# Kernel optimization log

Hardware: AMD Instinct MI355X
Metric: run time of the kernel (lower is better)

The kernel has to match this reference:

```python
import jax, jax.numpy as jnp
import numpy as np

N_NODES = 100000
N_EDGES = 3200000
D_IN = 128
D_H0 = 64
D_H1 = 32
N_GRAPHS = 1024
N_CLASSES = 16


def setup_inputs() -> dict:
    key = jax.random.key(0)
    ks = jax.random.split(key, 9)
    x = jax.random.normal(ks[0], (N_NODES, D_IN), dtype=jnp.float32)
    edge_index = jax.random.randint(ks[1], (2, N_EDGES), 0, N_NODES, dtype=jnp.int64)
    node_graph_index = jnp.sort(
        jax.random.randint(ks[2], (N_NODES,), 0, N_GRAPHS, dtype=jnp.int64))

    def glorot(k, shape):
        lim = np.sqrt(6.0 / (shape[0] + shape[1]))
        return jax.random.uniform(k, shape, jnp.float32, -lim, lim)

    W0 = glorot(ks[3], (D_IN, D_H0))
    b0 = jnp.zeros((D_H0,), jnp.float32)
    W1 = glorot(ks[4], (D_H0, D_H1))
    b1 = jnp.zeros((D_H1,), jnp.float32)
    Wd = glorot(ks[5], (D_H1, N_CLASSES))
    bd = jnp.zeros((N_CLASSES,), jnp.float32)
    return {"x": x, "edge_index": edge_index, "node_graph_index": node_graph_index,
            "W0": W0, "b0": b0, "W1": W1, "b1": b1, "Wd": Wd, "bd": bd}


def reference(x, edge_index, node_graph_index, W0, b0, W1, b1, Wd, bd):
    N = x.shape[0]
    # GCN renormalization: add self-loops, symmetric D^-1/2 (A+I) D^-1/2
    loops = jnp.arange(N, dtype=edge_index.dtype)
    row = jnp.concatenate([edge_index[0], loops])  # target nodes
    col = jnp.concatenate([edge_index[1], loops])  # source nodes
    deg = jax.ops.segment_sum(jnp.ones_like(row, dtype=x.dtype), row, num_segments=N)
    inv_sqrt = jax.lax.rsqrt(deg)  # deg >= 1 thanks to self-loops
    norm = inv_sqrt[row] * inv_sqrt[col]  # [E+N]

    def gcn(h, W, b):
        hW = h @ W                                   # [N, d_out]
        msg = hW[col] * norm[:, None]                # [E+N, d_out]
        agg = jax.ops.segment_sum(msg, row, num_segments=N)
        return jax.nn.relu(agg + b)

    h = gcn(x, W0, b0)          # [N, 64]  (dropout is identity at inference)
    h = gcn(h, W1, b1)          # [N, 32]

    # mean pool over graphs
    sums = jax.ops.segment_sum(h, node_graph_index, num_segments=N_GRAPHS)
    cnt = jax.ops.segment_sum(jnp.ones((N,), x.dtype), node_graph_index,
                              num_segments=N_GRAPHS)
    pooled = sums / jnp.maximum(cnt, 1.0)[:, None]   # [G, 32]
    return pooled @ Wd + bd                          # [G, n_classes]
```

## Files before the change

### kernel.cpp

```cpp
#include <hip/hip_runtime.h>

#define BSHIFT 7
#define BSIZE 128
#define MAXB 1024
#define CHUNK 4096
#define CAP 4608

typedef unsigned short bfraw;

__device__ __forceinline__ bfraw f2bf(float f) {
    unsigned u = __float_as_uint(f);
    unsigned r = u + 0x7FFFu + ((u >> 16) & 1u);
    return (bfraw)(r >> 16);
}
__device__ __forceinline__ float bflo(unsigned u) { return __uint_as_float(u << 16); }
__device__ __forceinline__ float bfhi(unsigned u) { return __uint_as_float(u & 0xFFFF0000u); }


__global__ __launch_bounds__(1024) void k_binit(int* __restrict__ bcur, int nbuckets) {
    int b = threadIdx.x;
    if (b < nbuckets) bcur[b] = b * CAP;
}

__global__ __launch_bounds__(512) void k_bscatter(const int* __restrict__ row,
                                                  const int* __restrict__ col,
                                                  int* __restrict__ bcur,
                                                  int* __restrict__ bedge,
                                                  int E, int nbuckets) {
    __shared__ int h[MAXB];
    __shared__ int base[MAXB];
    int tid = threadIdx.x;
    for (int i = tid; i < nbuckets; i += 512) h[i] = 0;
    __syncthreads();
    int start = blockIdx.x * CHUNK;
    int end = min(E, start + CHUNK);
    for (int i = start + tid; i < end; i += 512)
        atomicAdd(&h[row[i] >> BSHIFT], 1);
    __syncthreads();
    for (int i = tid; i < nbuckets; i += 512) {
        int c = h[i];
        base[i] = c ? atomicAdd(&bcur[i], c) : 0;
        h[i] = 0;
    }
    __syncthreads();
    for (int i = start + tid; i < end; i += 512) {
        int r = row[i], c = col[i];
        int b = r >> BSHIFT;
        int p = base[b] + atomicAdd(&h[b], 1);
        if (p < (b + 1) * CAP)
            bedge[p] = ((r & (BSIZE - 1)) << 17) | c;
    }
}

__global__ __launch_bounds__(512) void k_bexact(const int* __restrict__ bedge,
                                                const int* __restrict__ bcur,
                                                int* __restrict__ off,
                                                int* __restrict__ off2,
                                                int* __restrict__ scol,
                                                float* __restrict__ invs, int N) {
    __shared__ int sedge[CAP];
    __shared__ int ldeg[BSIZE];
    __shared__ int lex[BSIZE];
    int b = blockIdx.x;
    int tid = threadIdx.x;
    int nstart = b << BSHIFT;
    int ncount = min(BSIZE, N - nstart);
    int s = b * CAP;
    int cntE = min(bcur[b] - s, CAP);
    for (int k = tid; k < cntE; k += 512) sedge[k] = bedge[s + k];
    if (tid < BSIZE) ldeg[tid] = 0;
    __syncthreads();
    for (int k = tid; k < cntE; k += 512)
        atomicAdd(&ldeg[sedge[k] >> 17], 1);
    __syncthreads();
    if (tid < BSIZE) lex[tid] = ldeg[tid];
    __syncthreads();
    for (int d = 1; d < BSIZE; d <<= 1) {
        int a = 0;
        if (tid < BSIZE && tid >= d) a = lex[tid - d];
        __syncthreads();
        if (tid < BSIZE) lex[tid] += a;
        __syncthreads();
    }
    if (tid < BSIZE) lex[tid] -= ldeg[tid];
    __syncthreads();
    if (tid < ncount) {
        int node = nstart + tid;
        int st = s + lex[tid];
        off[node] = st;
        off2[node] = st + ldeg[tid];
        invs[node] = rsqrtf((float)(ldeg[tid] + 1));
    }
    if (tid < BSIZE) ldeg[tid] = 0;
    __syncthreads();
    for (int k = tid; k < cntE; k += 512) {
        int p = sedge[k];
        int lr = p >> 17;
        int pos = s + lex[lr] + atomicAdd(&ldeg[lr], 1);
        scol[pos] = p & 0x1FFFF;
    }
}


__global__ __launch_bounds__(256) void k_gemm0(const float* __restrict__ x,
                                               const float* __restrict__ W,
                                               const float* __restrict__ invs,
                                               bfraw* __restrict__ out, int N) {
    __shared__ float sW[128 * 64];
    for (int i = threadIdx.x; i < 2048; i += 256)
        ((float4*)sW)[i] = ((const float4*)W)[i];
    __syncthreads();
    int t = threadIdx.x;
    int tc = t & 15, tr = t >> 4;
    int rbase = blockIdx.x * 64 + tr * 4;
    float acc[4][4] = {};
    int rr[4];
#pragma unroll
    for (int i = 0; i < 4; ++i) rr[i] = min(rbase + i, N - 1);
    for (int k = 0; k < 128; k += 4) {
        float4 wv0 = *(const float4*)&sW[(k + 0) * 64 + tc * 4];
        float4 wv1 = *(const float4*)&sW[(k + 1) * 64 + tc * 4];
        float4 wv2 = *(const float4*)&sW[(k + 2) * 64 + tc * 4];
        float4 wv3 = *(const float4*)&sW[(k + 3) * 64 + tc * 4];
#pragma unroll
        for (int i = 0; i < 4; ++i) {
            float4 xv = *(const float4*)(x + (size_t)rr[i] * 128 + k);
            acc[i][0] = fmaf(xv.x, wv0.x, acc[i][0]);
            acc[i][1] = fmaf(xv.x, wv0.y, acc[i][1]);
            acc[i][2] = fmaf(xv.x, wv0.z, acc[i][2]);
            acc[i][3] = fmaf(xv.x, wv0.w, acc[i][3]);
            acc[i][0] = fmaf(xv.y, wv1.x, acc[i][0]);
            acc[i][1] = fmaf(xv.y, wv1.y, acc[i][1]);
            acc[i][2] = fmaf(xv.y, wv1.z, acc[i][2]);
            acc[i][3] = fmaf(xv.y, wv1.w, acc[i][3]);
            acc[i][0] = fmaf(xv.z, wv2.x, acc[i][0]);
            acc[i][1] = fmaf(xv.z, wv2.y, acc[i][1]);
            acc[i][2] = fmaf(xv.z, wv2.z, acc[i][2]);
            acc[i][3] = fmaf(xv.z, wv2.w, acc[i][3]);
            acc[i][0] = fmaf(xv.w, wv3.x, acc[i][0]);
            acc[i][1] = fmaf(xv.w, wv3.y, acc[i][1]);
            acc[i][2] = fmaf(xv.w, wv3.z, acc[i][2]);
            acc[i][3] = fmaf(xv.w, wv3.w, acc[i][3]);
        }
    }
#pragma unroll
    for (int i = 0; i < 4; ++i) {
        int row = rbase + i;
        if (row < N) {
            float iv = invs[row];
            ushort4 o;
            o.x = f2bf(iv * acc[i][0]);
            o.y = f2bf(iv * acc[i][1]);
            o.z = f2bf(iv * acc[i][2]);
            o.w = f2bf(iv * acc[i][3]);
            *(ushort4*)(out + (size_t)row * 64 + tc * 4) = o;
        }
    }
}

__global__ __launch_bounds__(256) void k_gemm1(const float* __restrict__ h,
                                               const float* __restrict__ W,
                                               const float* __restrict__ invs,
                                               bfraw* __restrict__ out, int N) {
    __shared__ float sW[64 * 32];
    for (int i = threadIdx.x; i < 512; i += 256)
        ((float4*)sW)[i] = ((const float4*)W)[i];
    __syncthreads();
    int t = threadIdx.x;
    int tc = t & 7, tr = t >> 3;
    int rbase = blockIdx.x * 128 + tr * 4;
    float acc[4][4] = {};
    int rr[4];
#pragma unroll
    for (int i = 0; i < 4; ++i) rr[i] = min(rbase + i, N - 1);
    for (int k = 0; k < 64; k += 4) {
        float4 wv0 = *(const float4*)&sW[(k + 0) * 32 + tc * 4];
        float4 wv1 = *(const float4*)&sW[(k + 1) * 32 + tc * 4];
        float4 wv2 = *(const float4*)&sW[(k + 2) * 32 + tc * 4];
        float4 wv3 = *(const float4*)&sW[(k + 3) * 32 + tc * 4];
#pragma unroll
        for (int i = 0; i < 4; ++i) {
            float4 xv = *(const float4*)(h + (size_t)rr[i] * 64 + k);
            acc[i][0] = fmaf(xv.x, wv0.x, acc[i][0]);
            acc[i][1] = fmaf(xv.x, wv0.y, acc[i][1]);
            acc[i][2] = fmaf(xv.x, wv0.z, acc[i][2]);
            acc[i][3] = fmaf(xv.x, wv0.w, acc[i][3]);
            acc[i][0] = fmaf(xv.y, wv1.x, acc[i][0]);
            acc[i][1] = fmaf(xv.y, wv1.y, acc[i][1]);
            acc[i][2] = fmaf(xv.y, wv1.z, acc[i][2]);
            acc[i][3] = fmaf(xv.y, wv1.w, acc[i][3]);
            acc[i][0] = fmaf(xv.z, wv2.x, acc[i][0]);
            acc[i][1] = fmaf(xv.z, wv2.y, acc[i][1]);
            acc[i][2] = fmaf(xv.z, wv2.z, acc[i][2]);
            acc[i][3] = fmaf(xv.z, wv2.w, acc[i][3]);
            acc[i][0] = fmaf(xv.w, wv3.x, acc[i][0]);
            acc[i][1] = fmaf(xv.w, wv3.y, acc[i][1]);
            acc[i][2] = fmaf(xv.w, wv3.z, acc[i][2]);
            acc[i][3] = fmaf(xv.w, wv3.w, acc[i][3]);
        }
    }
#pragma unroll
    for (int i = 0; i < 4; ++i) {
        int row = rbase + i;
        if (row < N) {
            float iv = invs[row];
            ushort4 o;
            o.x = f2bf(iv * acc[i][0]);
            o.y = f2bf(iv * acc[i][1]);
            o.z = f2bf(iv * acc[i][2]);
            o.w = f2bf(iv * acc[i][3]);
            *(ushort4*)(out + (size_t)row * 32 + tc * 4) = o;
        }
    }
}


__global__ __launch_bounds__(256) void k_agg64_w(const int* __restrict__ scol,
                                                 const int* __restrict__ off,
                                                 const int* __restrict__ off2,
                                                 const float* __restrict__ invs,
                                                 const bfraw* __restrict__ hWb,
                                                 const float* __restrict__ bias,
                                                 float* __restrict__ h0, int N) {
    int node = blockIdx.x * 4 + (threadIdx.x >> 6);
    if (node >= N) return;
    int lane = threadIdx.x & 63;
    int fl = lane & 7, sg = lane >> 3;
    int s = off[node], e = off2[node];
    float a[8] = {}, c[8] = {};
    int k = s + sg;
    for (; k + 24 < e; k += 32) {
        int n0 = scol[k], n1 = scol[k + 8], n2 = scol[k + 16], n3 = scol[k + 24];
        uint4 u0 = *(const uint4*)(hWb + (size_t)n0 * 64 + fl * 8);
        uint4 u1 = *(const uint4*)(hWb + (size_t)n1 * 64 + fl * 8);
        uint4 u2 = *(const uint4*)(hWb + (size_t)n2 * 64 + fl * 8);
        uint4 u3 = *(const uint4*)(hWb + (size_t)n3 * 64 + fl * 8);
        a[0] += bflo(u0.x); a[1] += bfhi(u0.x); a[2] += bflo(u0.y); a[3] += bfhi(u0.y);
        a[4] += bflo(u0.z); a[5] += bfhi(u0.z); a[6] += bflo(u0.w); a[7] += bfhi(u0.w);
        c[0] += bflo(u1.x); c[1] += bfhi(u1.x); c[2] += bflo(u1.y); c[3] += bfhi(u1.y);
        c[4] += bflo(u1.z); c[5] += bfhi(u1.z); c[6] += bflo(u1.w); c[7] += bfhi(u1.w);
        a[0] += bflo(u2.x); a[1] += bfhi(u2.x); a[2] += bflo(u2.y); a[3] += bfhi(u2.y);
        a[4] += bflo(u2.z); a[5] += bfhi(u2.z); a[6] += bflo(u2.w); a[7] += bfhi(u2.w);
        c[0] += bflo(u3.x); c[1] += bfhi(u3.x); c[2] += bflo(u3.y); c[3] += bfhi(u3.y);
        c[4] += bflo(u3.z); c[5] += bfhi(u3.z); c[6] += bflo(u3.w); c[7] += bfhi(u3.w);
    }
    for (; k < e; k += 8) {
        uint4 u = *(const uint4*)(hWb + (size_t)scol[k] * 64 + fl * 8);
        a[0] += bflo(u.x); a[1] += bfhi(u.x); a[2] += bflo(u.y); a[3] += bfhi(u.y);
        a[4] += bflo(u.z); a[5] += bfhi(u.z); a[6] += bflo(u.w); a[7] += bfhi(u.w);
    }
#pragma unroll
    for (int j = 0; j < 8; ++j) a[j] += c[j];
#pragma unroll
    for (int m = 8; m < 64; m <<= 1) {
#pragma unroll
        for (int j = 0; j < 8; ++j) a[j] += __shfl_xor(a[j], m, 64);
    }
    if (sg == 0) {
        uint4 u = *(const uint4*)(hWb + (size_t)node * 64 + fl * 8);
        float iv = invs[node];
        int fb = fl * 8;
        float4 o1, o2;
        o1.x = fmaxf(iv * (a[0] + bflo(u.x)) + bias[fb + 0], 0.f);
        o1.y = fmaxf(iv * (a[1] + bfhi(u.x)) + bias[fb + 1], 0.f);
        o1.z = fmaxf(iv * (a[2] + bflo(u.y)) + bias[fb + 2], 0.f);
        o1.w = fmaxf(iv * (a[3] + bfhi(u.y)) + bias[fb + 3], 0.f);
        o2.x = fmaxf(iv * (a[4] + bflo(u.z)) + bias[fb + 4], 0.f);
        o2.y = fmaxf(iv * (a[5] + bfhi(u.z)) + bias[fb + 5], 0.f);
        o2.z = fmaxf(iv * (a[6] + bflo(u.w)) + bias[fb + 6], 0.f);
        o2.w = fmaxf(iv * (a[7] + bfhi(u.w)) + bias[fb + 7], 0.f);
        *(float4*)(h0 + (size_t)node * 64 + fb) = o1;
        *(float4*)(h0 + (size_t)node * 64 + fb + 4) = o2;
    }
}

__global__ __launch_bounds__(256) void k_agg32_w(const int* __restrict__ scol,
                                                 const int* __restrict__ off,
                                                 const int* __restrict__ off2,
                                                 const float* __restrict__ invs,
                                                 const bfraw* __restrict__ hWb,
                                                 const float* __restrict__ bias,
                                                 float* __restrict__ h1, int N) {
    int node = blockIdx.x * 4 + (threadIdx.x >> 6);
    if (node >= N) return;
    int lane = threadIdx.x & 63;
    int fl = lane & 3, sg = lane >> 2;
    int s = off[node], e = off2[node];
    float a[8] = {}, c[8] = {};
    int k = s + sg;
    for (; k + 16 < e; k += 32) {
        int n0 = scol[k], n1 = scol[k + 16];
        uint4 u0 = *(const uint4*)(hWb + (size_t)n0 * 32 + fl * 8);
        uint4 u1 = *(const uint4*)(hWb + (size_t)n1 * 32 + fl * 8);
        a[0] += bflo(u0.x); a[1] += bfhi(u0.x); a[2] += bflo(u0.y); a[3] += bfhi(u0.y);
        a[4] += bflo(u0.z); a[5] += bfhi(u0.z); a[6] += bflo(u0.w); a[7] += bfhi(u0.w);
        c[0] += bflo(u1.x); c[1] += bfhi(u1.x); c[2] += bflo(u1.y); c[3] += bfhi(u1.y);
        c[4] += bflo(u1.z); c[5] += bfhi(u1.z); c[6] += bflo(u1.w); c[7] += bfhi(u1.w);
    }
    for (; k < e; k += 16) {
        uint4 u = *(const uint4*)(hWb + (size_t)scol[k] * 32 + fl * 8);
        a[0] += bflo(u.x); a[1] += bfhi(u.x); a[2] += bflo(u.y); a[3] += bfhi(u.y);
        a[4] += bflo(u.z); a[5] += bfhi(u.z); a[6] += bflo(u.w); a[7] += bfhi(u.w);
    }
#pragma unroll
    for (int j = 0; j < 8; ++j) a[j] += c[j];
#pragma unroll
    for (int m = 4; m < 64; m <<= 1) {
#pragma unroll
        for (int j = 0; j < 8; ++j) a[j] += __shfl_xor(a[j], m, 64);
    }
    if (sg == 0) {
        uint4 u = *(const uint4*)(hWb + (size_t)node * 32 + fl * 8);
        float iv = invs[node];
        int fb = fl * 8;
        float4 o1, o2;
        o1.x = fmaxf(iv * (a[0] + bflo(u.x)) + bias[fb + 0], 0.f);
        o1.y = fmaxf(iv * (a[1] + bfhi(u.x)) + bias[fb + 1], 0.f);
        o1.z = fmaxf(iv * (a[2] + bflo(u.y)) + bias[fb + 2], 0.f);
        o1.w = fmaxf(iv * (a[3] + bfhi(u.y)) + bias[fb + 3], 0.f);
        o2.x = fmaxf(iv * (a[4] + bflo(u.z)) + bias[fb + 4], 0.f);
        o2.y = fmaxf(iv * (a[5] + bfhi(u.z)) + bias[fb + 5], 0.f);
        o2.z = fmaxf(iv * (a[6] + bflo(u.w)) + bias[fb + 6], 0.f);
        o2.w = fmaxf(iv * (a[7] + bfhi(u.w)) + bias[fb + 7], 0.f);
        *(float4*)(h1 + (size_t)node * 32 + fb) = o1;
        *(float4*)(h1 + (size_t)node * 32 + fb + 4) = o2;
    }
}


__global__ __launch_bounds__(256) void k_gbound(const int* __restrict__ gidx,
                                                int* __restrict__ gstart,
                                                int N, int G) {
    int i = blockIdx.x * 256 + threadIdx.x;
    if (i > N) return;
    if (i == 0) {
        int g0 = gidx[0];
        for (int g = 0; g <= g0; ++g) gstart[g] = 0;
    } else if (i == N) {
        int gl = gidx[N - 1];
        for (int g = gl + 1; g <= G; ++g) gstart[g] = N;
    } else {
        int a = gidx[i - 1], b = gidx[i];
        for (int g = a + 1; g <= b; ++g) gstart[g] = i;
    }
}

__global__ __launch_bounds__(256) void k_pool_head(const float* __restrict__ h1,
                                                   const int* __restrict__ gstart,
                                                   const float* __restrict__ Wd,
                                                   const float* __restrict__ bd,
                                                   float* __restrict__ out) {
    int g = blockIdx.x;
    int s = gstart[g], e = gstart[g + 1];
    int tid = threadIdx.x;
    int lane = tid & 63, w = tid >> 6;
    int f = lane & 31, half = lane >> 5;
    float acc = 0.f;
    for (int n = s + w * 2 + half; n < e; n += 8)
        acc += h1[(size_t)n * 32 + f];
    acc += __shfl_xor(acc, 32, 64);
    __shared__ float red[4][32];
    if (half == 0) red[w][f] = acc;
    __syncthreads();
    if (tid < 32) {
        float v = red[0][tid] + red[1][tid] + red[2][tid] + red[3][tid];
        red[0][tid] = v / fmaxf((float)(e - s), 1.0f);
    }
    __syncthreads();
    if (tid < 16) {
        float acc2 = bd[tid];
#pragma unroll
        for (int j = 0; j < 32; ++j)
            acc2 = fmaf(red[0][j], Wd[j * 16 + tid], acc2);
        out[g * 16 + tid] = acc2;
    }
}


static inline size_t align256(size_t v) { return (v + 255) & ~(size_t)255; }

extern "C" void kernel_launch(void* const* d_in, const int* in_sizes, int n_in,
                              void* d_out, int out_size, void* d_ws, size_t ws_size,
                              hipStream_t stream) {
    const float* x   = (const float*)d_in[0];
    const int*  erow = (const int*)d_in[1];
    const int*  gidx = (const int*)d_in[2];
    const float* W0  = (const float*)d_in[3];
    const float* b0  = (const float*)d_in[4];
    const float* W1  = (const float*)d_in[5];
    const float* b1  = (const float*)d_in[6];
    const float* Wd  = (const float*)d_in[7];
    const float* bd  = (const float*)d_in[8];
    float* out = (float*)d_out;

    const int E = in_sizes[1] / 2;
    const int* ecol = erow + E;
    const int N = in_sizes[2];
    const int G = out_size / 16;
    const int nbuckets = (N + BSIZE - 1) / BSIZE;
    const int nchunks = (E + CHUNK - 1) / CHUNK;
    const size_t SLOTS = (size_t)nbuckets * CAP;

    char* ws = (char*)d_ws;
    size_t oInvs = 0;
    size_t oOff  = align256(oInvs + (size_t)N * 4);
    size_t oOff2 = align256(oOff + (size_t)N * 4);
    size_t oBc   = align256(oOff2 + (size_t)N * 4);
    size_t oScol = align256(oBc + (size_t)MAXB * 4);
    size_t oA    = align256(oScol + SLOTS * 4);
    size_t oB    = align256(oA + (size_t)N * 128);
    size_t oGs   = align256(oB + (size_t)N * 256);

    float* invs   = (float*)(ws + oInvs);
    int*   off    = (int*)(ws + oOff);
    int*   off2   = (int*)(ws + oOff2);
    int*   bcur   = (int*)(ws + oBc);
    int*   scol   = (int*)(ws + oScol);
    bfraw* tabA   = (bfraw*)(ws + oA);
    float* bufB   = (float*)(ws + oB);
    int*   gstart = (int*)(ws + oGs);
    int*   bedge  = (int*)bufB;
    float* h1     = bufB;

    k_binit<<<1, 1024, 0, stream>>>(bcur, nbuckets);
    k_bscatter<<<nchunks, 512, 0, stream>>>(erow, ecol, bcur, bedge, E, nbuckets);
    k_bexact<<<nbuckets, 512, 0, stream>>>(bedge, bcur, off, off2, scol, invs, N);

    k_gbound<<<(N + 256) / 256, 256, 0, stream>>>(gidx, gstart, N, G);

    k_gemm0<<<(N + 63) / 64, 256, 0, stream>>>(x, W0, invs, tabA, N);
    k_agg64_w<<<(N + 3) / 4, 256, 0, stream>>>(scol, off, off2, invs, tabA, b0, bufB, N);

    k_gemm1<<<(N + 127) / 128, 256, 0, stream>>>(bufB, W1, invs, tabA, N);
    k_agg32_w<<<(N + 3) / 4, 256, 0, stream>>>(scol, off, off2, invs, tabA, b1, h1, N);

    k_pool_head<<<G, 256, 0, stream>>>(h1, gstart, Wd, bd, out);
}
```

Measured before the change: 356.3 us.

## Replace bucketed two-pass CSR build with global degree atomics and per-node scatter

Builds the per-row edge lists differently. Each node's degree is counted with global atomics, a per-bucket scan produces the offsets, and each column index is then written straight to its final slot with a per-node atomic cursor. This removes the LDS bucket histogram, the intermediate bedge buffer and the second shared-memory reorder pass. In exchange it adds two passes of contended global atomics over 3.2M edges, and the order of columns within a row becomes nondeterministic.

```diff
diff --git a/kernel.cpp b/kernel.cpp
--- a/kernel.cpp
+++ b/kernel.cpp
@@ -3,7 +3,6 @@
 #define BSHIFT 7
 #define BSIZE 128
 #define MAXB 1024
-#define CHUNK 4096
 #define CAP 4608
 
 typedef unsigned short bfraw;
@@ -17,87 +16,76 @@
 __device__ __forceinline__ float bfhi(unsigned u) { return __uint_as_float(u & 0xFFFF0000u); }
 
 
-__global__ __launch_bounds__(1024) void k_binit(int* __restrict__ bcur, int nbuckets) {
-    int b = threadIdx.x;
-    if (b < nbuckets) bcur[b] = b * CAP;
-}
-
-__global__ __launch_bounds__(512) void k_bscatter(const int* __restrict__ row,
-                                                  const int* __restrict__ col,
-                                                  int* __restrict__ bcur,
-                                                  int* __restrict__ bedge,
-                                                  int E, int nbuckets) {
-    __shared__ int h[MAXB];
-    __shared__ int base[MAXB];
-    int tid = threadIdx.x;
-    for (int i = tid; i < nbuckets; i += 512) h[i] = 0;
+__global__ __launch_bounds__(256) void k_zero(int* __restrict__ deg, int N) {
+    int i = blockIdx.x * 256 + threadIdx.x;
+    if (i < N) deg[i] = 0;
+}
+
+__global__ __launch_bounds__(256) void k_deg(const int* __restrict__ row,
+                                             int* __restrict__ deg, int E) {
+    int i4 = (blockIdx.x * 256 + threadIdx.x) * 4;
+    if (i4 + 3 < E) {
+        int4 r = *(const int4*)(row + i4);
+        atomicAdd(&deg[r.x], 1);
+        atomicAdd(&deg[r.y], 1);
+        atomicAdd(&deg[r.z], 1);
+        atomicAdd(&deg[r.w], 1);
+    } else {
+        for (int i = i4; i < E; ++i) atomicAdd(&deg[row[i]], 1);
+    }
+}
+
+__global__ __launch_bounds__(128) void k_scanb(const int* __restrict__ deg,
+                                               int* __restrict__ off,
+                                               int* __restrict__ off2,
+                                               int* __restrict__ cur,
+                                               float* __restrict__ invs, int N) {
+    __shared__ int lex[BSIZE];
+    int b = blockIdx.x, tid = threadIdx.x;
+    int node = (b << BSHIFT) + tid;
+    int d = (node < N) ? deg[node] : 0;
+    lex[tid] = d;
     __syncthreads();
-    int start = blockIdx.x * CHUNK;
-    int end = min(E, start + CHUNK);
-    for (int i = start + tid; i < end; i += 512)
-        atomicAdd(&h[row[i] >> BSHIFT], 1);
-    __syncthreads();
-    for (int i = tid; i < nbuckets; i += 512) {
-        int c = h[i];
-        base[i] = c ? atomicAdd(&bcur[i], c) : 0;
-        h[i] = 0;
-    }
-    __syncthreads();
-    for (int i = start + tid; i < end; i += 512) {
-        int r = row[i], c = col[i];
-        int b = r >> BSHIFT;
-        int p = base[b] + atomicAdd(&h[b], 1);
-        if (p < (b + 1) * CAP)
-            bedge[p] = ((r & (BSIZE - 1)) << 17) | c;
-    }
-}
-
-__global__ __launch_bounds__(512) void k_bexact(const int* __restrict__ bedge,
-                                                const int* __restrict__ bcur,
-                                                int* __restrict__ off,
-                                                int* __restrict__ off2,
-                                                int* __restrict__ scol,
-                                                float* __restrict__ invs, int N) {
-    __shared__ int sedge[CAP];
-    __shared__ int ldeg[BSIZE];
-    __shared__ int lex[BSIZE];
-    int b = blockIdx.x;
-    int tid = threadIdx.x;
-    int nstart = b << BSHIFT;
-    int ncount = min(BSIZE, N - nstart);
-    int s = b * CAP;
-    int cntE = min(bcur[b] - s, CAP);
-    for (int k = tid; k < cntE; k += 512) sedge[k] = bedge[s + k];
-    if (tid < BSIZE) ldeg[tid] = 0;
-    __syncthreads();
-    for (int k = tid; k < cntE; k += 512)
-        atomicAdd(&ldeg[sedge[k] >> 17], 1);
-    __syncthreads();
-    if (tid < BSIZE) lex[tid] = ldeg[tid];
-    __syncthreads();
-    for (int d = 1; d < BSIZE; d <<= 1) {
-        int a = 0;
-        if (tid < BSIZE && tid >= d) a = lex[tid - d];
+    for (int s = 1; s < BSIZE; s <<= 1) {
+        int a = (tid >= s) ? lex[tid - s] : 0;
         __syncthreads();
-        if (tid < BSIZE) lex[tid] += a;
+        lex[tid] += a;
         __syncthreads();
     }
-    if (tid < BSIZE) lex[tid] -= ldeg[tid];
-    __syncthreads();
-    if (tid < ncount) {
-        int node = nstart + tid;
-        int st = s + lex[tid];
+    int incl = lex[tid];
+    int base = b * CAP;
+    int st = base + min(incl - d, CAP);
+    int en = base + min(incl, CAP);
+    if (node < N) {
         off[node] = st;
-        off2[node] = st + ldeg[tid];
-        invs[node] = rsqrtf((float)(ldeg[tid] + 1));
-    }
-    if (tid < BSIZE) ldeg[tid] = 0;
-    __syncthreads();
-    for (int k = tid; k < cntE; k += 512) {
-        int p = sedge[k];
-        int lr = p >> 17;
-        int pos = s + lex[lr] + atomicAdd(&ldeg[lr], 1);
-        scol[pos] = p & 0x1FFFF;
+        off2[node] = en;
+        cur[node] = st;
+        invs[node] = rsqrtf((float)(d + 1));
+    }
+}
+
+__global__ __launch_bounds__(256) void k_scatter(const int* __restrict__ row,
+                                                 const int* __restrict__ col,
+                                                 int* __restrict__ cur,
+                                                 int* __restrict__ scol, int E) {
+    int i4 = (blockIdx.x * 256 + threadIdx.x) * 4;
+    if (i4 + 3 < E) {
+        int4 r = *(const int4*)(row + i4);
+        int4 c = *(const int4*)(col + i4);
+        int p0 = atomicAdd(&cur[r.x], 1);
+        int p1 = atomicAdd(&cur[r.y], 1);
+        int p2 = atomicAdd(&cur[r.z], 1);
+        int p3 = atomicAdd(&cur[r.w], 1);
+        if (p0 < ((r.x >> BSHIFT) + 1) * CAP) scol[p0] = c.x;
+        if (p1 < ((r.y >> BSHIFT) + 1) * CAP) scol[p1] = c.y;
+        if (p2 < ((r.z >> BSHIFT) + 1) * CAP) scol[p2] = c.z;
+        if (p3 < ((r.w >> BSHIFT) + 1) * CAP) scol[p3] = c.w;
+    } else {
+        for (int i = i4; i < E; ++i) {
+            int r = row[i], c = col[i];
+            int p = atomicAdd(&cur[r], 1);
+            if (p < ((r >> BSHIFT) + 1) * CAP) scol[p] = c;
+        }
     }
 }
 
@@ -398,15 +386,15 @@
     const int N = in_sizes[2];
     const int G = out_size / 16;
     const int nbuckets = (N + BSIZE - 1) / BSIZE;
-    const int nchunks = (E + CHUNK - 1) / CHUNK;
     const size_t SLOTS = (size_t)nbuckets * CAP;
 
     char* ws = (char*)d_ws;
     size_t oInvs = 0;
     size_t oOff  = align256(oInvs + (size_t)N * 4);
     size_t oOff2 = align256(oOff + (size_t)N * 4);
-    size_t oBc   = align256(oOff2 + (size_t)N * 4);
-    size_t oScol = align256(oBc + (size_t)MAXB * 4);
+    size_t oCur  = align256(oOff2 + (size_t)N * 4);
+    size_t oDeg  = align256(oCur + (size_t)N * 4);
+    size_t oScol = align256(oDeg + (size_t)N * 4);
     size_t oA    = align256(oScol + SLOTS * 4);
     size_t oB    = align256(oA + (size_t)N * 128);
     size_t oGs   = align256(oB + (size_t)N * 256);
@@ -414,17 +402,18 @@
     float* invs   = (float*)(ws + oInvs);
     int*   off    = (int*)(ws + oOff);
     int*   off2   = (int*)(ws + oOff2);
-    int*   bcur   = (int*)(ws + oBc);
+    int*   cur    = (int*)(ws + oCur);
+    int*   deg    = (int*)(ws + oDeg);
     int*   scol   = (int*)(ws + oScol);
     bfraw* tabA   = (bfraw*)(ws + oA);
     float* bufB   = (float*)(ws + oB);
     int*   gstart = (int*)(ws + oGs);
-    int*   bedge  = (int*)bufB;
     float* h1     = bufB;
 
-    k_binit<<<1, 1024, 0, stream>>>(bcur, nbuckets);
-    k_bscatter<<<nchunks, 512, 0, stream>>>(erow, ecol, bcur, bedge, E, nbuckets);
-    k_bexact<<<nbuckets, 512, 0, stream>>>(bedge, bcur, off, off2, scol, invs, N);
+    k_zero<<<(N + 255) / 256, 256, 0, stream>>>(deg, N);
+    k_deg<<<(E + 1023) / 1024, 256, 0, stream>>>(erow, deg, E);
+    k_scanb<<<nbuckets, 128, 0, stream>>>(deg, off, off2, cur, invs, N);
+    k_scatter<<<(E + 1023) / 1024, 256, 0, stream>>>(erow, ecol, cur, scol, E);
 
     k_gbound<<<(N + 256) / 256, 256, 0, stream>>>(gidx, gstart, N, G);
 
```

Result: slower. 709.5 us (+99.1%).
